# Kernel tuning notes

Measured on AMD Instinct MI355X. Metric: run time of the kernel, lower is better.

The kernel has to match this reference:

```python
import jax, jax.numpy as jnp
import numpy as np

B, A, C, H, W = 4, 6, 80, 128, 128
INPUT_SHIFT = 4
IMG = 1024.0
K_PRE = 4095            # kSRamSize: pre-NMS candidate budget
POST_K = 300            # post_nms_top_k
THR_INT = 1             # ceil(0.05 * 2**INPUT_SHIFT)
NMS_THR = 128.0 / 256.0 # ceil(0.5 * 2**kNmsThresholdShift) / 2**8
MARGIN_INT = 0          # ceil(0.0 * 2**INPUT_SHIFT)
CLASS_OFFSET = 0
NEG = -(1 << 30)
OUT_SHIFT = 2           # kOutputBBoxShift


def setup_inputs() -> dict:
    key = jax.random.key(0)
    k1, = jax.random.split(key, 1)
    # quantized int8 repr (scale 1/2**4) of box deltas + class scores
    data = jax.random.randint(k1, (B, A * (4 + C), H, W), -128, 128, dtype=jnp.int32)
    # grid anchors: centers at stride 8, per-anchor square sizes
    stride = IMG / H
    ys, xs = np.meshgrid(np.arange(H), np.arange(W), indexing="ij")
    cx = ((xs + 0.5) * stride).astype(np.float32)
    cy = ((ys + 0.5) * stride).astype(np.float32)
    half = (32.0 * (1.33 ** np.arange(A, dtype=np.float32)))[:, None, None] / 2.0
    anchor = np.stack([cx[None] - half, cy[None] - half, cx[None] + half, cy[None] + half], axis=1)
    # exp table exactly as _gen_exp_table with in_scale = 1/2**INPUT_SHIFT
    idx = np.arange(-128, 128, dtype=np.float32) / (1 << INPUT_SHIFT)
    ev = np.exp(idx)
    bit_num = float(np.ceil(np.log2(ev.max() + 1.0)))
    exp_shift = int(max(15 - bit_num, INPUT_SHIFT))
    exp_table = np.round(ev * (1 << exp_shift)).astype(np.int32)
    return {"data": data, "anchor": jnp.asarray(anchor, jnp.float32),
            "exp_table": jnp.asarray(exp_table), "exp_shift": exp_shift}


def _decode(data, anchor, exp_table, exp_shift):
    d = data.reshape(B, A, 4 + C, H, W)
    deltas = jnp.transpose(d[:, :, :4], (0, 1, 3, 4, 2)).reshape(B, -1, 4)   # [B,N,4] int
    cls = jnp.transpose(d[:, :, 4:], (0, 1, 3, 4, 2)).reshape(B, -1, C)      # [B,N,C] int
    score = cls.max(-1)                                   # int, scale 1/2**4
    label = jnp.argmax(cls, -1).astype(jnp.int32) + CLASS_OFFSET
    anc = jnp.transpose(anchor, (0, 2, 3, 1)).reshape(-1, 4)                 # [N,4] matches (A,H,W)
    aw = anc[:, 2] - anc[:, 0]
    ah = anc[:, 3] - anc[:, 1]
    acx = (anc[:, 0] + anc[:, 2]) * 0.5
    acy = (anc[:, 1] + anc[:, 3]) * 0.5
    inv = 1.0 / (1 << INPUT_SHIFT)
    dx = deltas[..., 0].astype(jnp.float32) * inv
    dy = deltas[..., 1].astype(jnp.float32) * inv
    esc = 1.0 / (1 << exp_shift)
    ew = exp_table[jnp.clip(deltas[..., 2], -128, 127) + 128].astype(jnp.float32) * esc
    eh = exp_table[jnp.clip(deltas[..., 3], -128, 127) + 128].astype(jnp.float32) * esc
    pcx = acx + dx * aw
    pcy = acy + dy * ah
    pw = aw * ew
    ph = ah * eh
    boxes = jnp.stack([pcx - pw * 0.5, pcy - ph * 0.5, pcx + pw * 0.5, pcy + ph * 0.5], -1)
    return jnp.clip(boxes, 0.0, IMG), score, label       # use_clippings


def _iou(b):  # [K,4] -> [K,K]
    area = jnp.maximum(b[:, 2] - b[:, 0], 0.0) * jnp.maximum(b[:, 3] - b[:, 1], 0.0)
    lt = jnp.maximum(b[:, None, :2], b[None, :, :2])
    rb = jnp.minimum(b[:, None, 2:], b[None, :, 2:])
    wh = jnp.maximum(rb - lt, 0.0)
    inter = wh[..., 0] * wh[..., 1]
    return inter / jnp.maximum(area[:, None] + area[None, :] - inter, 1e-6)


def _nms(boxes, scores, labels):
    # boxes/scores are pre-sorted by descending score
    sup = (_iou(boxes) > NMS_THR) \
          & (labels[:, None] == labels[None, :]) \
          & ((scores[:, None] - scores[None, :]) >= MARGIN_INT)
    valid = scores > NEG
    idx = jnp.arange(K_PRE)

    def body(i, keep):
        sup_i = sup[i] & (idx > i)
        return jnp.where(keep[i] & valid[i], keep & jnp.logical_not(sup_i), keep)

    return jax.lax.fori_loop(0, K_PRE, body, valid)


def reference(data, anchor, exp_table, exp_shift):
    boxes, score, label = _decode(data, anchor, exp_table, exp_shift)
    ms = jnp.where(score >= THR_INT, score, NEG)          # box_filter_threshold
    topv, topi = jax.lax.top_k(ms, K_PRE)                 # [B,K]
    boxes_k = jnp.take_along_axis(boxes, topi[:, :, None], axis=1)
    labels_k = jnp.take_along_axis(label, topi, axis=1)
    keep = jax.vmap(_nms)(boxes_k, topv, labels_k)
    fs = jnp.where(keep, topv, NEG)
    outv, outi = jax.lax.top_k(fs, POST_K)
    out_boxes = jnp.take_along_axis(boxes_k, outi[:, :, None], axis=1)
    out_labels = jnp.take_along_axis(labels_k, outi, axis=1)
    out_boxes_i = jnp.round(out_boxes * (1 << OUT_SHIFT)).astype(jnp.int32)  # qint16 @ kOutputBBoxShift
    return out_boxes_i, outv.astype(jnp.int32), out_labels
```

## Files before the change

kernel.cpp:

```cpp
#include <hip/hip_runtime.h>
#include <stdint.h>

#define BATCH 4
#define NA 6
#define NC 80
#define HW (128*128)
#define NPB (NA*HW)
#define KPRE 4095
#define KPAD 4096
#define POSTK 300
#define NEGV (-(1<<30))
#define NCHUNK (NPB/256)
#define R1 1024

#define OFF_BOXES    0
#define OFF_BOXK     6291456
#define OFF_MS       6553600
#define OFF_LAB      8126464
#define OFF_BCNT     9699328
#define OFF_BASE     10485760
#define OFF_SCUT     10487808
#define OFF_TOT      10487872
#define OFF_TOPV     10489920
#define OFF_LABK     10555456
#define OFF_MASK     10620992

__device__ __forceinline__ float4 dpp_decode_box(int dxi, int dyi, int dwi, int dhi,
                                                 float a0, float a1, float a2, float a3,
                                                 const int* __restrict__ exp_table, float esc) {
#pragma clang fp contract(off)
    float aw  = a2 - a0;
    float ah  = a3 - a1;
    float acx = (a0 + a2) * 0.5f;
    float acy = (a1 + a3) * 0.5f;
    float dx  = (float)dxi * 0.0625f;
    float dy  = (float)dyi * 0.0625f;
    int e2 = dwi < -128 ? -128 : (dwi > 127 ? 127 : dwi);
    int e3 = dhi < -128 ? -128 : (dhi > 127 ? 127 : dhi);
    float ew = (float)exp_table[e2 + 128] * esc;
    float eh = (float)exp_table[e3 + 128] * esc;
    float pcx = acx + dx * aw;
    float pcy = acy + dy * ah;
    float pw = aw * ew;
    float ph = ah * eh;
    float x0 = pcx - pw * 0.5f;
    float y0 = pcy - ph * 0.5f;
    float x1 = pcx + pw * 0.5f;
    float y1 = pcy + ph * 0.5f;
    x0 = fminf(fmaxf(x0, 0.f), 1024.f);
    y0 = fminf(fmaxf(y0, 0.f), 1024.f);
    x1 = fminf(fmaxf(x1, 0.f), 1024.f);
    y1 = fminf(fmaxf(y1, 0.f), 1024.f);
    return make_float4(x0, y0, x1, y1);
}

__device__ __forceinline__ bool dpp_sup_test(float4 p, float pa, int pl_, float4 c, int cl_) {
#pragma clang fp contract(off)
    float cw = fmaxf(c.z - c.x, 0.f), ch = fmaxf(c.w - c.y, 0.f);
    float ca = cw * ch;
    float lx = fmaxf(p.x, c.x), ly = fmaxf(p.y, c.y);
    float rx = fminf(p.z, c.z), ry = fminf(p.w, c.w);
    float wx = fmaxf(rx - lx, 0.f), wy = fmaxf(ry - ly, 0.f);
    float inter = wx * wy;
    float uni = fmaxf((pa + ca) - inter, 1e-6f);
    float iou = inter / uni;
    return (iou > 0.5f) && (cl_ == pl_);
}

__global__ __launch_bounds__(256) void dpp_decode_kernel(
        const int* __restrict__ data, const float* __restrict__ anchor,
        const int* __restrict__ exp_table, const int* __restrict__ exp_shift_p,
        int* __restrict__ ms, int* __restrict__ labels, float4* __restrict__ boxes,
        int* __restrict__ blockcnt) {
    int b = blockIdx.z, a = blockIdx.y, tid = threadIdx.x;
    int idx = blockIdx.x * 256 + tid;
    const int4* dptr = (const int4*)(data + (size_t)(b * NA + a) * 84 * HW);

    int4 d0 = dptr[idx];
    int4 d1 = dptr[4096 + idx];
    int4 d2 = dptr[2 * 4096 + idx];
    int4 d3 = dptr[3 * 4096 + idx];

    int4 m = dptr[4 * 4096 + idx];
    int4 lab = make_int4(0, 0, 0, 0);
#pragma unroll 4
    for (int c = 1; c < NC; c++) {
        int4 v = dptr[(4 + c) * 4096 + idx];
        if (v.x > m.x) { m.x = v.x; lab.x = c; }
        if (v.y > m.y) { m.y = v.y; lab.y = c; }
        if (v.z > m.z) { m.z = v.z; lab.z = c; }
        if (v.w > m.w) { m.w = v.w; lab.w = c; }
    }

    const float4* aptr = (const float4*)(anchor + (size_t)a * 4 * HW);
    float4 ax0 = aptr[idx];
    float4 ay0 = aptr[4096 + idx];
    float4 ax1 = aptr[2 * 4096 + idx];
    float4 ay1 = aptr[3 * 4096 + idx];

    int eshift = exp_shift_p[0];
    float esc = 1.0f / (float)(1 << eshift);

    float4 box0 = dpp_decode_box(d0.x, d1.x, d2.x, d3.x, ax0.x, ay0.x, ax1.x, ay1.x, exp_table, esc);
    float4 box1 = dpp_decode_box(d0.y, d1.y, d2.y, d3.y, ax0.y, ay0.y, ax1.y, ay1.y, exp_table, esc);
    float4 box2 = dpp_decode_box(d0.z, d1.z, d2.z, d3.z, ax0.z, ay0.z, ax1.z, ay1.z, exp_table, esc);
    float4 box3 = dpp_decode_box(d0.w, d1.w, d2.w, d3.w, ax0.w, ay0.w, ax1.w, ay1.w, exp_table, esc);

    int s0 = (m.x >= 1) ? m.x : NEGV;
    int s1 = (m.y >= 1) ? m.y : NEGV;
    int s2 = (m.z >= 1) ? m.z : NEGV;
    int s3 = (m.w >= 1) ? m.w : NEGV;

    size_t nb = (size_t)b * NPB + (size_t)a * HW;
    ((int4*)ms)[(nb >> 2) + idx] = make_int4(s0, s1, s2, s3);
    ((int4*)labels)[(nb >> 2) + idx] = lab;
    boxes[nb + 4 * (size_t)idx]     = box0;
    boxes[nb + 4 * (size_t)idx + 1] = box1;
    boxes[nb + 4 * (size_t)idx + 2] = box2;
    boxes[nb + 4 * (size_t)idx + 3] = box3;

    __shared__ int hist[512];
    hist[tid] = 0;
    hist[tid + 256] = 0;
    __syncthreads();
    int q = tid >> 6;
    if (s0 >= 1) atomicAdd(&hist[q * 128 + s0], 1);
    if (s1 >= 1) atomicAdd(&hist[q * 128 + s1], 1);
    if (s2 >= 1) atomicAdd(&hist[q * 128 + s2], 1);
    if (s3 >= 1) atomicAdd(&hist[q * 128 + s3], 1);
    __syncthreads();
#pragma unroll
    for (int k = 0; k < 2; k++) {
        int lin = tid + (k << 8);
        int q2 = lin >> 7, v = lin & 127;
        int chunk = a * 64 + blockIdx.x * 4 + q2;
        blockcnt[((b << 7) + v) * NCHUNK + chunk] = hist[q2 * 128 + v];
    }
}

__global__ __launch_bounds__(384) void dpp_scan_kernel(int* __restrict__ bcnt,
                                                       int* __restrict__ tot,
                                                       int* __restrict__ topv,
                                                       int* __restrict__ labk,
                                                       float4* __restrict__ boxk) {
    int v = blockIdx.x, b = blockIdx.y, t = threadIdx.x;
    if (t < 32) {
        int slot = (b << 12) + (v << 5) + t;
        topv[slot] = NEGV;
        labk[slot] = 0;
        boxk[slot] = make_float4(0.f, 0.f, 0.f, 0.f);
    }
    int* bc = bcnt + ((b << 7) + v) * NCHUNK;
    int x = bc[t];
    int lane = t & 63, w = t >> 6;
    int s = x;
#pragma unroll
    for (int d = 1; d < 64; d <<= 1) {
        int y = __shfl_up(s, d);
        if (lane >= d) s += y;
    }
    __shared__ int wsum[6];
    if (lane == 63) wsum[w] = s;
    __syncthreads();
    int off = 0;
    for (int i = 0; i < w; i++) off += wsum[i];
    int incl = s + off;
    bc[t] = incl - x;
    if (t == NCHUNK - 1) tot[(b << 7) + v] = incl;
}

__global__ __launch_bounds__(512) void dpp_cutoff_kernel(const int* __restrict__ tot,
                                                         int* __restrict__ base,
                                                         int* __restrict__ s_cut) {
    int t = threadIdx.x;
    int b = t >> 7, v = t & 127;
    __shared__ int lds[512];
    lds[t] = tot[t];
    __syncthreads();
    if (v == 0) {
        int cum = 0, sc = 1;
        for (int vv = 127; vv >= 1; vv--) {
            base[(b << 7) + vv] = cum;
            cum += lds[(b << 7) + vv];
            sc = vv;
            if (cum >= KPRE) break;
        }
        s_cut[b] = sc;
    }
}

__global__ __launch_bounds__(256) void dpp_place_kernel(
        const int* __restrict__ ms, const int* __restrict__ labels, const float4* __restrict__ boxes,
        const int* __restrict__ blockoff, const int* __restrict__ base, const int* __restrict__ s_cut,
        int* __restrict__ topv, int* __restrict__ labk, float4* __restrict__ boxk) {
    int chunk = blockIdx.x, b = blockIdx.y, tid = threadIdx.x;
    int lane = tid & 63, w = tid >> 6;
    int n = (chunk << 8) + tid;
    int s = ms[(size_t)b * NPB + n];

    __shared__ int whist[512];
    whist[tid] = 0;
    whist[tid + 256] = 0;
    __syncthreads();
    if (s >= 1) atomicAdd(&whist[(w << 7) + s], 1);

    unsigned long long eq = ~0ull;
#pragma unroll
    for (int k = 0; k < 7; k++) {
        unsigned long long bk = __ballot((s >> k) & 1);
        eq &= ((s >> k) & 1) ? bk : ~bk;
    }
    int r = __popcll(eq & ((1ull << lane) - 1ull));
    __syncthreads();

    int sc = s_cut[b];
    if (s >= sc) {
        for (int w2 = 0; w2 < w; w2++) r += whist[(w2 << 7) + s];
        int pos = base[(b << 7) + s] + blockoff[((b << 7) + s) * NCHUNK + chunk] + r;
        if (pos < KPRE) {
            topv[(b << 12) + pos] = s;
            labk[(b << 12) + pos] = labels[(size_t)b * NPB + n];
            boxk[(b << 12) + pos] = boxes[(size_t)b * NPB + n];
        }
    }
}

__global__ __launch_bounds__(256) void dpp_mask_kernel(
        const float4* __restrict__ boxk, const int* __restrict__ labk,
        unsigned long long* __restrict__ mask) {
#pragma clang fp contract(off)
    int cc = blockIdx.x, rg = blockIdx.y, b = blockIdx.z;
    int t = threadIdx.x, lane = t & 63;
    int rc = (rg << 2) + (t >> 6);
    int row = (rc << 6) + lane;
    __shared__ float4 cb[64];
    __shared__ int cl[64];
    int col0 = cc << 6;
    if (t < 64) {
        cb[t] = boxk[(b << 12) + col0 + t];
        cl[t] = labk[(b << 12) + col0 + t];
    }
    __syncthreads();
    size_t mi = ((size_t)b * R1 + row) * 64 + cc;
    if (cc < rc) {
        mask[mi] = 0ull;
        return;
    }
    float4 rbx = boxk[(b << 12) + row];
    int rl = labk[(b << 12) + row];
    float rw = fmaxf(rbx.z - rbx.x, 0.f), rh = fmaxf(rbx.w - rbx.y, 0.f);
    float ra = rw * rh;
    unsigned long long bits = 0ull;
#pragma unroll 4
    for (int j = 0; j < 64; j++) {
        bool sup = dpp_sup_test(rbx, ra, rl, cb[j], cl[j]) && ((col0 + j) > row);
        if (sup) bits |= (1ull << j);
    }
    mask[mi] = bits;
}

__global__ __launch_bounds__(64) void dpp_nms_kernel(
        const float4* __restrict__ boxk, const int* __restrict__ labk, const int* __restrict__ topv,
        const unsigned long long* __restrict__ mask, int* __restrict__ out) {
#pragma clang fp contract(off)
    int b = blockIdx.x, lane = threadIdx.x;
    const int* tv = topv + (b << 12);
    const unsigned long long* mrow = mask + (size_t)b * R1 * 64;

    unsigned long long sup = 0ull;
    for (int k = 0; k < 64; k++) {
        int v = tv[(k << 6) + lane];
        unsigned long long mb = __ballot(v <= NEGV);
        if (lane == k) sup = mb;
    }

    __shared__ int keep_lds[POSTK];
    int kc = 0;
    unsigned long long w_win = __shfl(sup, 0);

    unsigned long long pl[8], pu[8];
#pragma unroll
    for (int u = 0; u < 8; u++) {
        pl[u] = mrow[(size_t)u * 64 + lane];
        pu[u] = mrow[(size_t)u * 64 + 0];
    }

    bool done = false;
    for (int ii = 0; ii < R1 && !done; ii += 8) {
#pragma unroll
        for (int u = 0; u < 8; u++) {
            int i = ii + u;
            if (!done) {
                if ((i & 63) == 0 && i != 0) w_win = __shfl(sup, i >> 6);
                if (!((w_win >> (i & 63)) & 1ull)) {
                    if (lane == 0) keep_lds[kc] = i;
                    kc++;
                    if (kc == POSTK) {
                        done = true;
                    } else {
                        sup   |= pl[u];
                        w_win |= pu[u];
                    }
                }
            }
            int r = i + 8;
            if (r > R1 - 1) r = R1 - 1;
            pl[u] = mrow[(size_t)r * 64 + lane];
            pu[u] = mrow[(size_t)r * 64 + (r >> 6)];
        }
    }

    if (kc < POSTK) {
        for (int i = R1; i < KPRE && kc < POSTK; i++) {
            unsigned long long w = __shfl(sup, i >> 6);
            if ((w >> (i & 63)) & 1ull) continue;
            float4 bi = boxk[(b << 12) + i];
            int li = labk[(b << 12) + i];
            bool supp = false;
            for (int k = lane; k < kc; k += 64) {
                int j = keep_lds[k];
                float4 c = boxk[(b << 12) + j];
                float cw = fmaxf(c.z - c.x, 0.f), ch = fmaxf(c.w - c.y, 0.f);
                float ca = cw * ch;
                supp |= dpp_sup_test(c, ca, labk[(b << 12) + j], bi, li);
            }
            if (__ballot(supp)) {
                if (lane == (i >> 6)) sup |= 1ull << (i & 63);
            } else {
                if (lane == 0) keep_lds[kc] = i;
                kc++;
            }
        }
    }

    int kept = kc;
    if (kc < POSTK) {
        for (int j = 0; j < KPRE && kc < POSTK; j++) {
            unsigned long long w = __shfl(sup, j >> 6);
            if ((w >> (j & 63)) & 1ull) {
                if (lane == 0) keep_lds[kc] = j;
                kc++;
            }
        }
    }
    __syncthreads();

    for (int k = lane; k < POSTK; k += 64) {
        int slot = keep_lds[k];
        float4 bx = boxk[(b << 12) + slot];
        int lb = labk[(b << 12) + slot];
        int sv = (k < kept) ? tv[slot] : NEGV;
        int o = ((b * POSTK) + k) << 2;
        out[o + 0] = (int)rintf(bx.x * 4.0f);
        out[o + 1] = (int)rintf(bx.y * 4.0f);
        out[o + 2] = (int)rintf(bx.z * 4.0f);
        out[o + 3] = (int)rintf(bx.w * 4.0f);
        out[BATCH * POSTK * 4 + b * POSTK + k] = sv;
        out[BATCH * POSTK * 5 + b * POSTK + k] = lb;
    }
}

extern "C" void kernel_launch(void* const* d_in, const int* in_sizes, int n_in,
                              void* d_out, int out_size, void* d_ws, size_t ws_size,
                              hipStream_t stream) {
    const int*   data      = (const int*)d_in[0];
    const float* anchor    = (const float*)d_in[1];
    const int*   exp_table = (const int*)d_in[2];
    const int*   exp_shift = (const int*)d_in[3];

    char* ws = (char*)d_ws;
    float4* boxes  = (float4*)(ws + OFF_BOXES);
    float4* boxk   = (float4*)(ws + OFF_BOXK);
    int*    ms     = (int*)(ws + OFF_MS);
    int*    labels = (int*)(ws + OFF_LAB);
    int*    bcnt   = (int*)(ws + OFF_BCNT);
    int*    base   = (int*)(ws + OFF_BASE);
    int*    s_cut  = (int*)(ws + OFF_SCUT);
    int*    tot    = (int*)(ws + OFF_TOT);
    int*    topv   = (int*)(ws + OFF_TOPV);
    int*    labk   = (int*)(ws + OFF_LABK);
    unsigned long long* mask = (unsigned long long*)(ws + OFF_MASK);

    dpp_decode_kernel<<<dim3(16, NA, BATCH), 256, 0, stream>>>(
        data, anchor, exp_table, exp_shift, ms, labels, boxes, bcnt);
    dpp_scan_kernel<<<dim3(128, BATCH), 384, 0, stream>>>(bcnt, tot, topv, labk, boxk);
    dpp_cutoff_kernel<<<1, 512, 0, stream>>>(tot, base, s_cut);
    dpp_place_kernel<<<dim3(NCHUNK, BATCH), 256, 0, stream>>>(
        ms, labels, boxes, bcnt, base, s_cut, topv, labk, boxk);
    dpp_mask_kernel<<<dim3(64, 4, BATCH), 256, 0, stream>>>(boxk, labk, mask);
    dpp_nms_kernel<<<BATCH, 64, 0, stream>>>(boxk, labk, topv, mask, (int*)d_out);
}
```

Baseline: 265.1 us.

## Defer box decode to placed candidates and pack score with label

```diff
diff --git a/kernel.cpp b/kernel.cpp
--- a/kernel.cpp
+++ b/kernel.cpp
@@ -7,23 +7,20 @@
 #define HW (128*128)
 #define NPB (NA*HW)
 #define KPRE 4095
-#define KPAD 4096
 #define POSTK 300
 #define NEGV (-(1<<30))
 #define NCHUNK (NPB/256)
 #define R1 1024
 
-#define OFF_BOXES    0
-#define OFF_BOXK     6291456
-#define OFF_MS       6553600
-#define OFF_LAB      8126464
-#define OFF_BCNT     9699328
-#define OFF_BASE     10485760
-#define OFF_SCUT     10487808
-#define OFF_TOT      10487872
-#define OFF_TOPV     10489920
-#define OFF_LABK     10555456
-#define OFF_MASK     10620992
+#define OFF_MS       0
+#define OFF_BCNT     1572864
+#define OFF_BASE     2359296
+#define OFF_SCUT     2361344
+#define OFF_TOT      2361536
+#define OFF_TOPV     2363584
+#define OFF_LABK     2429120
+#define OFF_BOXK     2494656
+#define OFF_MASK     2756800
 
 __device__ __forceinline__ float4 dpp_decode_box(int dxi, int dyi, int dwi, int dhi,
                                                  float a0, float a1, float a2, float a3,
@@ -67,19 +64,14 @@
     return (iou > 0.5f) && (cl_ == pl_);
 }
 
-__global__ __launch_bounds__(256) void dpp_decode_kernel(
-        const int* __restrict__ data, const float* __restrict__ anchor,
-        const int* __restrict__ exp_table, const int* __restrict__ exp_shift_p,
-        int* __restrict__ ms, int* __restrict__ labels, float4* __restrict__ boxes,
-        int* __restrict__ blockcnt) {
-    int b = blockIdx.z, a = blockIdx.y, tid = threadIdx.x;
-    int idx = blockIdx.x * 256 + tid;
+__global__ __launch_bounds__(192) void dpp_decode_kernel(
+        const int* __restrict__ data, int* __restrict__ ms, int* __restrict__ blockcnt) {
+    int blk = blockIdx.x, tid = threadIdx.x;
+    int b = blk >> 7;
+    int g_in_b = (blk & 127) * 192 + tid;
+    int a = g_in_b >> 12;
+    int idx = g_in_b & 4095;
     const int4* dptr = (const int4*)(data + (size_t)(b * NA + a) * 84 * HW);
-
-    int4 d0 = dptr[idx];
-    int4 d1 = dptr[4096 + idx];
-    int4 d2 = dptr[2 * 4096 + idx];
-    int4 d3 = dptr[3 * 4096 + idx];
 
     int4 m = dptr[4 * 4096 + idx];
     int4 lab = make_int4(0, 0, 0, 0);
@@ -92,49 +84,29 @@
         if (v.w > m.w) { m.w = v.w; lab.w = c; }
     }
 
-    const float4* aptr = (const float4*)(anchor + (size_t)a * 4 * HW);
-    float4 ax0 = aptr[idx];
-    float4 ay0 = aptr[4096 + idx];
-    float4 ax1 = aptr[2 * 4096 + idx];
-    float4 ay1 = aptr[3 * 4096 + idx];
-
-    int eshift = exp_shift_p[0];
-    float esc = 1.0f / (float)(1 << eshift);
-
-    float4 box0 = dpp_decode_box(d0.x, d1.x, d2.x, d3.x, ax0.x, ay0.x, ax1.x, ay1.x, exp_table, esc);
-    float4 box1 = dpp_decode_box(d0.y, d1.y, d2.y, d3.y, ax0.y, ay0.y, ax1.y, ay1.y, exp_table, esc);
-    float4 box2 = dpp_decode_box(d0.z, d1.z, d2.z, d3.z, ax0.z, ay0.z, ax1.z, ay1.z, exp_table, esc);
-    float4 box3 = dpp_decode_box(d0.w, d1.w, d2.w, d3.w, ax0.w, ay0.w, ax1.w, ay1.w, exp_table, esc);
-
-    int s0 = (m.x >= 1) ? m.x : NEGV;
-    int s1 = (m.y >= 1) ? m.y : NEGV;
-    int s2 = (m.z >= 1) ? m.z : NEGV;
-    int s3 = (m.w >= 1) ? m.w : NEGV;
-
-    size_t nb = (size_t)b * NPB + (size_t)a * HW;
-    ((int4*)ms)[(nb >> 2) + idx] = make_int4(s0, s1, s2, s3);
-    ((int4*)labels)[(nb >> 2) + idx] = lab;
-    boxes[nb + 4 * (size_t)idx]     = box0;
-    boxes[nb + 4 * (size_t)idx + 1] = box1;
-    boxes[nb + 4 * (size_t)idx + 2] = box2;
-    boxes[nb + 4 * (size_t)idx + 3] = box3;
-
-    __shared__ int hist[512];
+    int p0 = (m.x >= 1) ? ((m.x << 7) | lab.x) : NEGV;
+    int p1 = (m.y >= 1) ? ((m.y << 7) | lab.y) : NEGV;
+    int p2 = (m.z >= 1) ? ((m.z << 7) | lab.z) : NEGV;
+    int p3 = (m.w >= 1) ? ((m.w << 7) | lab.w) : NEGV;
+
+    ((int4*)ms)[(size_t)b * (NPB / 4) + g_in_b] = make_int4(p0, p1, p2, p3);
+
+    __shared__ int hist[384];
     hist[tid] = 0;
-    hist[tid + 256] = 0;
+    if (tid < 192) hist[tid + 192] = 0;
     __syncthreads();
     int q = tid >> 6;
-    if (s0 >= 1) atomicAdd(&hist[q * 128 + s0], 1);
-    if (s1 >= 1) atomicAdd(&hist[q * 128 + s1], 1);
-    if (s2 >= 1) atomicAdd(&hist[q * 128 + s2], 1);
-    if (s3 >= 1) atomicAdd(&hist[q * 128 + s3], 1);
-    __syncthreads();
+    if (m.x >= 1) atomicAdd(&hist[q * 128 + m.x], 1);
+    if (m.y >= 1) atomicAdd(&hist[q * 128 + m.y], 1);
+    if (m.z >= 1) atomicAdd(&hist[q * 128 + m.z], 1);
+    if (m.w >= 1) atomicAdd(&hist[q * 128 + m.w], 1);
+    __syncthreads();
+    int chunk0 = (blk & 127) * 3;
 #pragma unroll
     for (int k = 0; k < 2; k++) {
-        int lin = tid + (k << 8);
+        int lin = tid + 192 * k;
         int q2 = lin >> 7, v = lin & 127;
-        int chunk = a * 64 + blockIdx.x * 4 + q2;
-        blockcnt[((b << 7) + v) * NCHUNK + chunk] = hist[q2 * 128 + v];
+        blockcnt[((b << 7) + v) * NCHUNK + chunk0 + q2] = hist[q2 * 128 + v];
     }
 }
 
@@ -190,13 +162,16 @@
 }
 
 __global__ __launch_bounds__(256) void dpp_place_kernel(
-        const int* __restrict__ ms, const int* __restrict__ labels, const float4* __restrict__ boxes,
-        const int* __restrict__ blockoff, const int* __restrict__ base, const int* __restrict__ s_cut,
+        const int* __restrict__ data, const float* __restrict__ anchor,
+        const int* __restrict__ exp_table, const int* __restrict__ exp_shift_p,
+        const int* __restrict__ ms, const int* __restrict__ blockoff,
+        const int* __restrict__ base, const int* __restrict__ s_cut,
         int* __restrict__ topv, int* __restrict__ labk, float4* __restrict__ boxk) {
     int chunk = blockIdx.x, b = blockIdx.y, tid = threadIdx.x;
     int lane = tid & 63, w = tid >> 6;
     int n = (chunk << 8) + tid;
-    int s = ms[(size_t)b * NPB + n];
+    int packed = ms[(size_t)b * NPB + n];
+    int s = packed >> 7;
 
     __shared__ int whist[512];
     whist[tid] = 0;
@@ -218,9 +193,22 @@
         for (int w2 = 0; w2 < w; w2++) r += whist[(w2 << 7) + s];
         int pos = base[(b << 7) + s] + blockoff[((b << 7) + s) * NCHUNK + chunk] + r;
         if (pos < KPRE) {
+            int a2 = n >> 14, p2 = n & (HW - 1);
+            const int* dp = data + ((size_t)(b * NA + a2) * 84) * HW + p2;
+            int d0 = dp[0];
+            int d1 = dp[HW];
+            int d2 = dp[2 * HW];
+            int d3 = dp[3 * HW];
+            const float* ap = anchor + (size_t)(a2 * 4) * HW + p2;
+            float a0 = ap[0];
+            float a1 = ap[HW];
+            float a3v = ap[2 * HW];
+            float a4v = ap[3 * HW];
+            float esc = 1.0f / (float)(1 << exp_shift_p[0]);
+            float4 box = dpp_decode_box(d0, d1, d2, d3, a0, a1, a3v, a4v, exp_table, esc);
             topv[(b << 12) + pos] = s;
-            labk[(b << 12) + pos] = labels[(size_t)b * NPB + n];
-            boxk[(b << 12) + pos] = boxes[(size_t)b * NPB + n];
+            labk[(b << 12) + pos] = packed & 127;
+            boxk[(b << 12) + pos] = box;
         }
     }
 }
@@ -369,24 +357,21 @@
     const int*   exp_shift = (const int*)d_in[3];
 
     char* ws = (char*)d_ws;
-    float4* boxes  = (float4*)(ws + OFF_BOXES);
-    float4* boxk   = (float4*)(ws + OFF_BOXK);
     int*    ms     = (int*)(ws + OFF_MS);
-    int*    labels = (int*)(ws + OFF_LAB);
     int*    bcnt   = (int*)(ws + OFF_BCNT);
     int*    base   = (int*)(ws + OFF_BASE);
     int*    s_cut  = (int*)(ws + OFF_SCUT);
     int*    tot    = (int*)(ws + OFF_TOT);
     int*    topv   = (int*)(ws + OFF_TOPV);
     int*    labk   = (int*)(ws + OFF_LABK);
+    float4* boxk   = (float4*)(ws + OFF_BOXK);
     unsigned long long* mask = (unsigned long long*)(ws + OFF_MASK);
 
-    dpp_decode_kernel<<<dim3(16, NA, BATCH), 256, 0, stream>>>(
-        data, anchor, exp_table, exp_shift, ms, labels, boxes, bcnt);
+    dpp_decode_kernel<<<512, 192, 0, stream>>>(data, ms, bcnt);
     dpp_scan_kernel<<<dim3(128, BATCH), 384, 0, stream>>>(bcnt, tot, topv, labk, boxk);
     dpp_cutoff_kernel<<<1, 512, 0, stream>>>(tot, base, s_cut);
     dpp_place_kernel<<<dim3(NCHUNK, BATCH), 256, 0, stream>>>(
-        ms, labels, boxes, bcnt, base, s_cut, topv, labk, boxk);
+        data, anchor, exp_table, exp_shift, ms, bcnt, base, s_cut, topv, labk, boxk);
     dpp_mask_kernel<<<dim3(64, 4, BATCH), 256, 0, stream>>>(boxk, labk, mask);
     dpp_nms_kernel<<<BATCH, 64, 0, stream>>>(boxk, labk, topv, mask, (int*)d_out);
 }
```

Result: slower. 272.6 us (+2.8%).

## Pack score+label, fold cutoff into place kernel, stage NMS diagonal in LDS

Applied to the files above, without the earlier changes.

```diff
diff --git a/kernel.cpp b/kernel.cpp
--- a/kernel.cpp
+++ b/kernel.cpp
@@ -7,23 +7,20 @@
 #define HW (128*128)
 #define NPB (NA*HW)
 #define KPRE 4095
-#define KPAD 4096
 #define POSTK 300
 #define NEGV (-(1<<30))
 #define NCHUNK (NPB/256)
 #define R1 1024
 
 #define OFF_BOXES    0
-#define OFF_BOXK     6291456
-#define OFF_MS       6553600
-#define OFF_LAB      8126464
-#define OFF_BCNT     9699328
-#define OFF_BASE     10485760
-#define OFF_SCUT     10487808
-#define OFF_TOT      10487872
-#define OFF_TOPV     10489920
-#define OFF_LABK     10555456
-#define OFF_MASK     10620992
+#define OFF_MS       6291456
+#define OFF_BCNT     7864320
+#define OFF_TOT      8650752
+#define OFF_TOPV     8652800
+#define OFF_LABK     8718336
+#define OFF_BOXK     8783872
+#define OFF_MASK     9046016
+#define OFF_DIAG     11143168
 
 __device__ __forceinline__ float4 dpp_decode_box(int dxi, int dyi, int dwi, int dhi,
                                                  float a0, float a1, float a2, float a3,
@@ -70,8 +67,7 @@
 __global__ __launch_bounds__(256) void dpp_decode_kernel(
         const int* __restrict__ data, const float* __restrict__ anchor,
         const int* __restrict__ exp_table, const int* __restrict__ exp_shift_p,
-        int* __restrict__ ms, int* __restrict__ labels, float4* __restrict__ boxes,
-        int* __restrict__ blockcnt) {
+        int* __restrict__ ms, float4* __restrict__ boxes, int* __restrict__ blockcnt) {
     int b = blockIdx.z, a = blockIdx.y, tid = threadIdx.x;
     int idx = blockIdx.x * 256 + tid;
     const int4* dptr = (const int4*)(data + (size_t)(b * NA + a) * 84 * HW);
@@ -106,14 +102,13 @@
     float4 box2 = dpp_decode_box(d0.z, d1.z, d2.z, d3.z, ax0.z, ay0.z, ax1.z, ay1.z, exp_table, esc);
     float4 box3 = dpp_decode_box(d0.w, d1.w, d2.w, d3.w, ax0.w, ay0.w, ax1.w, ay1.w, exp_table, esc);
 
-    int s0 = (m.x >= 1) ? m.x : NEGV;
-    int s1 = (m.y >= 1) ? m.y : NEGV;
-    int s2 = (m.z >= 1) ? m.z : NEGV;
-    int s3 = (m.w >= 1) ? m.w : NEGV;
+    int p0 = (m.x >= 1) ? ((m.x << 7) | lab.x) : NEGV;
+    int p1 = (m.y >= 1) ? ((m.y << 7) | lab.y) : NEGV;
+    int p2 = (m.z >= 1) ? ((m.z << 7) | lab.z) : NEGV;
+    int p3 = (m.w >= 1) ? ((m.w << 7) | lab.w) : NEGV;
 
     size_t nb = (size_t)b * NPB + (size_t)a * HW;
-    ((int4*)ms)[(nb >> 2) + idx] = make_int4(s0, s1, s2, s3);
-    ((int4*)labels)[(nb >> 2) + idx] = lab;
+    ((int4*)ms)[(nb >> 2) + idx] = make_int4(p0, p1, p2, p3);
     boxes[nb + 4 * (size_t)idx]     = box0;
     boxes[nb + 4 * (size_t)idx + 1] = box1;
     boxes[nb + 4 * (size_t)idx + 2] = box2;
@@ -124,10 +119,10 @@
     hist[tid + 256] = 0;
     __syncthreads();
     int q = tid >> 6;
-    if (s0 >= 1) atomicAdd(&hist[q * 128 + s0], 1);
-    if (s1 >= 1) atomicAdd(&hist[q * 128 + s1], 1);
-    if (s2 >= 1) atomicAdd(&hist[q * 128 + s2], 1);
-    if (s3 >= 1) atomicAdd(&hist[q * 128 + s3], 1);
+    if (m.x >= 1) atomicAdd(&hist[q * 128 + m.x], 1);
+    if (m.y >= 1) atomicAdd(&hist[q * 128 + m.y], 1);
+    if (m.z >= 1) atomicAdd(&hist[q * 128 + m.z], 1);
+    if (m.w >= 1) atomicAdd(&hist[q * 128 + m.w], 1);
     __syncthreads();
 #pragma unroll
     for (int k = 0; k < 2; k++) {
@@ -169,39 +164,36 @@
     if (t == NCHUNK - 1) tot[(b << 7) + v] = incl;
 }
 
-__global__ __launch_bounds__(512) void dpp_cutoff_kernel(const int* __restrict__ tot,
-                                                         int* __restrict__ base,
-                                                         int* __restrict__ s_cut) {
-    int t = threadIdx.x;
-    int b = t >> 7, v = t & 127;
-    __shared__ int lds[512];
-    lds[t] = tot[t];
-    __syncthreads();
-    if (v == 0) {
-        int cum = 0, sc = 1;
-        for (int vv = 127; vv >= 1; vv--) {
-            base[(b << 7) + vv] = cum;
-            cum += lds[(b << 7) + vv];
-            sc = vv;
-            if (cum >= KPRE) break;
-        }
-        s_cut[b] = sc;
-    }
-}
-
 __global__ __launch_bounds__(256) void dpp_place_kernel(
-        const int* __restrict__ ms, const int* __restrict__ labels, const float4* __restrict__ boxes,
-        const int* __restrict__ blockoff, const int* __restrict__ base, const int* __restrict__ s_cut,
+        const int* __restrict__ ms, const float4* __restrict__ boxes,
+        const int* __restrict__ blockoff, const int* __restrict__ tot,
         int* __restrict__ topv, int* __restrict__ labk, float4* __restrict__ boxk) {
     int chunk = blockIdx.x, b = blockIdx.y, tid = threadIdx.x;
     int lane = tid & 63, w = tid >> 6;
-    int n = (chunk << 8) + tid;
-    int s = ms[(size_t)b * NPB + n];
-
+
+    __shared__ int lds_tot[128];
+    __shared__ int lds_base[128];
+    __shared__ int lds_sc;
     __shared__ int whist[512];
+    if (tid < 128) lds_tot[tid] = tot[(b << 7) + tid];
     whist[tid] = 0;
     whist[tid + 256] = 0;
-    __syncthreads();
+
+    int n = (chunk << 8) + tid;
+    int packed = ms[(size_t)b * NPB + n];
+    int s = packed >> 7;
+    __syncthreads();
+
+    if (tid == 0) {
+        int cum = 0, sc = 1;
+        for (int vv = 127; vv >= 1; vv--) {
+            lds_base[vv] = cum;
+            cum += lds_tot[vv];
+            sc = vv;
+            if (cum >= KPRE) break;
+        }
+        lds_sc = sc;
+    }
     if (s >= 1) atomicAdd(&whist[(w << 7) + s], 1);
 
     unsigned long long eq = ~0ull;
@@ -213,13 +205,13 @@
     int r = __popcll(eq & ((1ull << lane) - 1ull));
     __syncthreads();
 
-    int sc = s_cut[b];
+    int sc = lds_sc;
     if (s >= sc) {
         for (int w2 = 0; w2 < w; w2++) r += whist[(w2 << 7) + s];
-        int pos = base[(b << 7) + s] + blockoff[((b << 7) + s) * NCHUNK + chunk] + r;
+        int pos = lds_base[s] + blockoff[((b << 7) + s) * NCHUNK + chunk] + r;
         if (pos < KPRE) {
             topv[(b << 12) + pos] = s;
-            labk[(b << 12) + pos] = labels[(size_t)b * NPB + n];
+            labk[(b << 12) + pos] = packed & 127;
             boxk[(b << 12) + pos] = boxes[(size_t)b * NPB + n];
         }
     }
@@ -227,7 +219,7 @@
 
 __global__ __launch_bounds__(256) void dpp_mask_kernel(
         const float4* __restrict__ boxk, const int* __restrict__ labk,
-        unsigned long long* __restrict__ mask) {
+        unsigned long long* __restrict__ mask, unsigned long long* __restrict__ diag) {
 #pragma clang fp contract(off)
     int cc = blockIdx.x, rg = blockIdx.y, b = blockIdx.z;
     int t = threadIdx.x, lane = t & 63;
@@ -257,15 +249,22 @@
         if (sup) bits |= (1ull << j);
     }
     mask[mi] = bits;
+    if (cc == rc) diag[(size_t)b * R1 + row] = bits;
 }
 
 __global__ __launch_bounds__(64) void dpp_nms_kernel(
         const float4* __restrict__ boxk, const int* __restrict__ labk, const int* __restrict__ topv,
-        const unsigned long long* __restrict__ mask, int* __restrict__ out) {
+        const unsigned long long* __restrict__ mask, const unsigned long long* __restrict__ diag,
+        int* __restrict__ out) {
 #pragma clang fp contract(off)
     int b = blockIdx.x, lane = threadIdx.x;
     const int* tv = topv + (b << 12);
     const unsigned long long* mrow = mask + (size_t)b * R1 * 64;
+
+    __shared__ unsigned long long pu_lds[R1];
+    __shared__ int keep_lds[POSTK];
+    for (int r2 = lane; r2 < R1; r2 += 64)
+        pu_lds[r2] = diag[(size_t)b * R1 + r2];
 
     unsigned long long sup = 0ull;
     for (int k = 0; k < 64; k++) {
@@ -273,20 +272,24 @@
         unsigned long long mb = __ballot(v <= NEGV);
         if (lane == k) sup = mb;
     }
-
-    __shared__ int keep_lds[POSTK];
+    __syncthreads();
+
     int kc = 0;
     unsigned long long w_win = __shfl(sup, 0);
 
-    unsigned long long pl[8], pu[8];
-#pragma unroll
-    for (int u = 0; u < 8; u++) {
-        pl[u] = mrow[(size_t)u * 64 + lane];
-        pu[u] = mrow[(size_t)u * 64 + 0];
-    }
+    unsigned long long pl[3][8];
+#pragma unroll
+    for (int g = 0; g < 3; g++)
+#pragma unroll
+        for (int u = 0; u < 8; u++)
+            pl[g][u] = mrow[(size_t)(g * 8 + u) * 64 + lane];
 
     bool done = false;
     for (int ii = 0; ii < R1 && !done; ii += 8) {
+        int g = (ii >> 3) % 3;
+        unsigned long long pur[8];
+#pragma unroll
+        for (int u = 0; u < 8; u++) pur[u] = pu_lds[ii + u];
 #pragma unroll
         for (int u = 0; u < 8; u++) {
             int i = ii + u;
@@ -298,15 +301,14 @@
                     if (kc == POSTK) {
                         done = true;
                     } else {
-                        sup   |= pl[u];
-                        w_win |= pu[u];
+                        sup   |= pl[g][u];
+                        w_win |= pur[u];
                     }
                 }
             }
-            int r = i + 8;
+            int r = ii + 24 + u;
             if (r > R1 - 1) r = R1 - 1;
-            pl[u] = mrow[(size_t)r * 64 + lane];
-            pu[u] = mrow[(size_t)r * 64 + (r >> 6)];
+            pl[g][u] = mrow[(size_t)r * 64 + lane];
         }
     }
 
@@ -370,23 +372,20 @@
 
     char* ws = (char*)d_ws;
     float4* boxes  = (float4*)(ws + OFF_BOXES);
-    float4* boxk   = (float4*)(ws + OFF_BOXK);
     int*    ms     = (int*)(ws + OFF_MS);
-    int*    labels = (int*)(ws + OFF_LAB);
     int*    bcnt   = (int*)(ws + OFF_BCNT);
-    int*    base   = (int*)(ws + OFF_BASE);
-    int*    s_cut  = (int*)(ws + OFF_SCUT);
     int*    tot    = (int*)(ws + OFF_TOT);
     int*    topv   = (int*)(ws + OFF_TOPV);
     int*    labk   = (int*)(ws + OFF_LABK);
+    float4* boxk   = (float4*)(ws + OFF_BOXK);
     unsigned long long* mask = (unsigned long long*)(ws + OFF_MASK);
+    unsigned long long* diag = (unsigned long long*)(ws + OFF_DIAG);
 
     dpp_decode_kernel<<<dim3(16, NA, BATCH), 256, 0, stream>>>(
-        data, anchor, exp_table, exp_shift, ms, labels, boxes, bcnt);
+        data, anchor, exp_table, exp_shift, ms, boxes, bcnt);
     dpp_scan_kernel<<<dim3(128, BATCH), 384, 0, stream>>>(bcnt, tot, topv, labk, boxk);
-    dpp_cutoff_kernel<<<1, 512, 0, stream>>>(tot, base, s_cut);
     dpp_place_kernel<<<dim3(NCHUNK, BATCH), 256, 0, stream>>>(
-        ms, labels, boxes, bcnt, base, s_cut, topv, labk, boxk);
-    dpp_mask_kernel<<<dim3(64, 4, BATCH), 256, 0, stream>>>(boxk, labk, mask);
-    dpp_nms_kernel<<<BATCH, 64, 0, stream>>>(boxk, labk, topv, mask, (int*)d_out);
-}
+        ms, boxes, bcnt, tot, topv, labk, boxk);
+    dpp_mask_kernel<<<dim3(64, 4, BATCH), 256, 0, stream>>>(boxk, labk, mask, diag);
+    dpp_nms_kernel<<<BATCH, 64, 0, stream>>>(boxk, labk, topv, mask, diag, (int*)d_out);
+}
```

After: 364.2 us. +37.4%, slower.
